# Optimization experiments

Measured on AMD Instinct MI355X. Metric: run time of the kernel, lower is better.

## Reference

```python
import jax, jax.numpy as jnp
import numpy as np

N_ITER = 3
B, L, U = 32, 120, 640
INPUT_CAPS = 32 * 9 * 12  # 3456
N_CLASSES = 5
FINAL_DIM = 16
N_REL = 25


def squash(x):
    # x: (B, n_caps, dim); squash along dim (axis=2)
    l2 = jnp.sum(x * x, axis=2, keepdims=True)
    return x * (l2 / (1.0 + l2) / jnp.sqrt(l2))


def conv2d(x, w, b, stride):
    out = jax.lax.conv_general_dilated(
        x, w, window_strides=stride, padding='VALID',
        dimension_numbers=('NCHW', 'OIHW', 'NCHW'))
    return out + b[None, :, None, None]


def setup_inputs() -> dict:
    key = jax.random.key(0)
    ks = jax.random.split(key, 10)
    stdv = 1.0 / np.sqrt(INPUT_CAPS)
    return {
        'input': jax.random.normal(ks[0], (B, 1, L, U), jnp.float32),
        'conv1_w': jax.random.normal(ks[1], (256, 1, L // 4, U // 4), jnp.float32) * 0.02,
        'conv1_b': jnp.zeros((256,), jnp.float32),
        'prim_w': jax.random.normal(ks[2], (256, 256, 10, 10), jnp.float32) * 0.02,
        'prim_b': jnp.zeros((256,), jnp.float32),
        'caps_w': jax.random.uniform(ks[3], (INPUT_CAPS, 8, N_CLASSES * FINAL_DIM),
                                     jnp.float32, -stdv, stdv),
        'b_route': jnp.zeros((INPUT_CAPS, N_CLASSES), jnp.float32),
        'pred_w': jax.random.normal(ks[4], (N_REL, FINAL_DIM), jnp.float32) * 0.1,
        'pred_b': jnp.zeros((N_REL,), jnp.float32),
        'eos_w': jax.random.normal(ks[5], (1, FINAL_DIM), jnp.float32) * 0.1,
        'eos_b': jnp.zeros((1,), jnp.float32),
    }


def reference(input, conv1_w, conv1_b, prim_w, prim_b, caps_w, b_route,
              pred_w, pred_b, eos_w, eos_b):
    # conv1 + relu: (B,1,120,640) -> (B,256,91,121)
    x = jax.nn.relu(conv2d(input, conv1_w, conv1_b, (1, 4)))
    # primary caps conv: -> (B,256,9,12)
    out = conv2d(x, prim_w, prim_b, (10, 10))
    n, _, h, w = out.shape
    out = out.reshape(n, 32, 8, h, w)                 # (B,32,8,9,12)
    out = jnp.transpose(out, (0, 1, 3, 4, 2))         # (B,32,9,12,8)
    u = squash(out.reshape(n, -1, 8))                 # (B,3456,8)
    # caps layer prediction: (B,I,8) x (I,8,O*D) -> (B,I,O,D)
    u_predict = jnp.einsum('bic,icj->bij', u, caps_w)
    u_predict = u_predict.reshape(n, INPUT_CAPS, N_CLASSES, FINAL_DIM)
    # agreement routing
    c = jax.nn.softmax(b_route, axis=1)               # (I,O)
    s = jnp.einsum('io,biod->bod', c, u_predict)
    v = squash(s)
    b_batch = jnp.broadcast_to(b_route, (n, INPUT_CAPS, N_CLASSES))
    for _ in range(N_ITER):
        b_batch = b_batch + jnp.einsum('biod,bod->bio', u_predict, v)
        c = jax.nn.softmax(b_batch, axis=-1)          # (B,I,O)
        s = jnp.einsum('bio,biod->bod', c, u_predict)
        v = squash(s)                                 # (B,O,D)
    predict_logits = v @ pred_w.T + pred_b            # (B,O,25)
    eos_logits = v @ eos_w.T + eos_b                  # (B,O,1)
    logits = jnp.concatenate([predict_logits, eos_logits], axis=-1)
    return jax.nn.log_softmax(logits, axis=-1)
```

## Files before the change

kernel.cpp:

```cpp
#include <hip/hip_runtime.h>

typedef __bf16 bf16x8 __attribute__((ext_vector_type(8)));
typedef __bf16 bf16x4 __attribute__((ext_vector_type(4)));
typedef float  f32x4  __attribute__((ext_vector_type(4)));
typedef unsigned int  uint;
typedef unsigned short ushort_t;

static __device__ __forceinline__ ushort_t f2bf(float f) {
    uint u = __float_as_uint(f);
    return (ushort_t)((u + 0x7fffu + ((u >> 16) & 1u)) >> 16);
}
static __device__ __forceinline__ float bf2f(ushort_t u) {
    return __uint_as_float((uint)u << 16);
}
static __device__ __forceinline__ f32x4 up4(uint2 p) {
    f32x4 r;
    r[0] = __uint_as_float(p.x << 16);
    r[1] = __uint_as_float(p.x & 0xffff0000u);
    r[2] = __uint_as_float(p.y << 16);
    r[3] = __uint_as_float(p.y & 0xffff0000u);
    return r;
}


constexpr size_t OFF_W1F = 0;
constexpr size_t SZ_W1F  = (size_t)256 * 4800 * 2;
constexpr size_t OFF_A2  = OFF_W1F + SZ_W1F;
constexpr size_t SZ_A2   = (size_t)256 * 25600 * 2;
constexpr size_t OFF_X   = OFF_A2 + SZ_A2;
constexpr size_t SZ_X    = (size_t)32 * 90 * 120 * 256 * 2;
constexpr size_t OFF_P   = OFF_X + SZ_X;
constexpr size_t SZ_P    = (size_t)8 * 256 * 32 * 112 * 2;
constexpr size_t OFF_UP  = OFF_X;
constexpr size_t OFF_BB  = OFF_X + (size_t)24 * 1024 * 1024;
constexpr size_t OFF_S0  = OFF_X + (size_t)28 * 1024 * 1024;
constexpr size_t OFF_S1  = OFF_X + (size_t)29 * 1024 * 1024;
constexpr size_t WS_NEED = OFF_P + SZ_P;

__global__ void k0_w1(const float* __restrict__ w, ushort_t* __restrict__ o) {
    int t = blockIdx.x * 256 + threadIdx.x;
    int l   = t & 63;
    int q   = t >> 6;
    int kwc = q % 5;
    int ocb = (q / 5) % 16;
    int kh  = q / 80;
    const float* src = w + (size_t)(ocb * 16 + (l & 15)) * 4800 + kh * 160 + kwc * 32 + (l >> 4) * 8;
    float4 f0 = *(const float4*)src;
    float4 f1 = *(const float4*)(src + 4);
    uint4 pk;
    pk.x = (uint)f2bf(f0.x) | ((uint)f2bf(f0.y) << 16);
    pk.y = (uint)f2bf(f0.z) | ((uint)f2bf(f0.w) << 16);
    pk.z = (uint)f2bf(f1.x) | ((uint)f2bf(f1.y) << 16);
    pk.w = (uint)f2bf(f1.z) | ((uint)f2bf(f1.w) << 16);
    *(uint4*)&o[(size_t)t * 8] = pk;
}

__global__ void k0_a2(const float* __restrict__ w, ushort_t* __restrict__ o) {
    __shared__ ushort_t l[25600];
    int oc2 = blockIdx.x;
    const float* src = w + (size_t)oc2 * 25600;
    for (int idx = threadIdx.x; idx < 25600; idx += 256) l[idx] = f2bf(src[idx]);
    __syncthreads();
    ushort_t* dst = o + (size_t)oc2 * 25600;
    for (int idx = threadIdx.x; idx < 25600; idx += 256) {
        int p = idx >> 8, ic = idx & 255;
        dst[idx] = l[ic * 100 + p];
    }
}

__global__ __launch_bounds__(256, 2) void k1_conv1(const float* __restrict__ inp,
                                                   const ushort_t* __restrict__ w1f,
                                                   const float* __restrict__ cb,
                                                   ushort_t* __restrict__ X) {
    __shared__ ushort_t smem[31680];
    ushort_t* brow = smem;
    const int tid = threadIdx.x, lane = tid & 63, wid = tid >> 6;
    const int wm = wid * 64;
    const int h = blockIdx.x, b = blockIdx.y;
    const int l16 = lane & 15, g8 = (lane >> 4) * 8;
    const int bbase = 4 * l16 + g8;
    f32x4 acc[4][8] = {};

    for (int idx = tid; idx < 5280; idx += 256) {
        int r = idx / 176, c = idx % 176;
        uint2 pk; pk.x = 0u; pk.y = 0u;
        if (c < 160) {
            const float* irow = inp + ((size_t)b * 120 + h + r) * 640;
            float4 f = *(const float4*)&irow[c * 4];
            pk.x = (uint)f2bf(f.x) | ((uint)f2bf(f.y) << 16);
            pk.y = (uint)f2bf(f.z) | ((uint)f2bf(f.w) << 16);
        }
        *(uint2*)&brow[r * 704 + c * 4] = pk;
    }
    __syncthreads();

#pragma unroll 1
    for (int kh = 0; kh < 30; ++kh) {
        bf16x8 bc[19];
        const int rb = kh * 704 + bbase;
#pragma unroll
        for (int t = 0; t < 19; ++t) {
            union { bf16x8 v8; bf16x4 v4[2]; } fr;
            fr.v4[0] = *(const bf16x4*)&brow[rb + 32 * t];
            fr.v4[1] = *(const bf16x4*)&brow[rb + 32 * t + 4];
            bc[t] = fr.v8;
        }
#pragma unroll
        for (int kwc = 0; kwc < 5; ++kwc) {
            bf16x8 af[4];
#pragma unroll
            for (int mt = 0; mt < 4; ++mt) {
                int q = (kh * 16 + wid * 4 + mt) * 5 + kwc;
                af[mt] = *(const bf16x8*)&w1f[(size_t)q * 512 + lane * 8];
            }
#pragma unroll
            for (int nt = 0; nt < 8; ++nt)
#pragma unroll
                for (int mt = 0; mt < 4; ++mt)
                    acc[mt][nt] = __builtin_amdgcn_mfma_f32_16x16x32_bf16(af[mt], bc[2 * nt + kwc], acc[mt][nt], 0, 0, 0);
        }
    }

    float cbv[4][4];
#pragma unroll
    for (int mt = 0; mt < 4; ++mt)
#pragma unroll
        for (int r = 0; r < 4; ++r)
            cbv[mt][r] = cb[wm + mt * 16 + (lane >> 4) * 4 + r];
    __syncthreads();
    ushort_t* cs = smem;
#pragma unroll
    for (int nt = 0; nt < 8; ++nt) {
        int wg = nt * 16 + l16;
        if (wg < 120) {
#pragma unroll
            for (int mt = 0; mt < 4; ++mt)
#pragma unroll
                for (int r = 0; r < 4; ++r) {
                    int oc = wm + mt * 16 + (lane >> 4) * 4 + r;
                    float v = acc[mt][nt][r] + cbv[mt][r];
                    v = v > 0.f ? v : 0.f;
                    cs[wg * 264 + oc] = f2bf(v);
                }
        }
    }
    __syncthreads();
    ushort_t* Xbase = X + ((size_t)b * 90 + h) * 120 * 256;
    for (int idx = tid; idx < 3840; idx += 256) {
        int w = idx >> 5, c = (idx & 31) * 8;
        *(uint4*)&Xbase[(size_t)w * 256 + c] = *(const uint4*)&cs[w * 264 + c];
    }
}

__global__ __launch_bounds__(512) void k2_prim(const ushort_t* __restrict__ X,
                                               const ushort_t* __restrict__ A2,
                                               ushort_t* __restrict__ P) {
    __shared__ float red[4][64][57];
    const int tid = threadIdx.x, lane = tid & 63, wid = tid >> 6;
    const int half = wid >> 2, ws2 = wid & 3;
    const int mi = blockIdx.x, s = blockIdx.y, b = blockIdx.z;
    const int msub = mi * 128 + ws2 * 32;
    const int l16 = lane & 15, g8 = (lane >> 4) * 8;
    f32x4 acc[2][7] = {};
    size_t aoff[2];
#pragma unroll
    for (int t = 0; t < 2; ++t) aoff[t] = (size_t)(msub + t * 16 + l16) * 25600 + g8;
    size_t noff[7];
#pragma unroll
    for (int nt = 0; nt < 7; ++nt) {
        int n = nt * 16 + l16; n = n < 108 ? n : 107;
        int h2 = n / 12, w2 = n % 12;
        noff[nt] = (((size_t)b * 90 + 10 * h2) * 120 + 10 * w2) * 256 + g8;
    }
    const int pbeg = (100 * s) / 8, pend = (100 * (s + 1)) / 8;
    const int pmid = pbeg + (pend - pbeg + 1) / 2;
    const int p0 = half ? pmid : pbeg;
    const int p1 = half ? pend : pmid;
#pragma unroll 1
    for (int p = p0; p < p1; ++p) {
        int ph = p / 10, pw = p % 10;
        size_t xb = (size_t)(ph * 120 + pw) * 256;
        size_t ab = (size_t)p * 256;
#pragma unroll
        for (int icc = 0; icc < 8; ++icc) {
            bf16x8 af[2], bfr[7];
#pragma unroll
            for (int t = 0; t < 2; ++t)
                af[t] = *(const bf16x8*)&A2[aoff[t] + ab + icc * 32];
#pragma unroll
            for (int nt = 0; nt < 7; ++nt)
                bfr[nt] = *(const bf16x8*)&X[noff[nt] + xb + icc * 32];
#pragma unroll
            for (int t = 0; t < 2; ++t)
#pragma unroll
                for (int nt = 0; nt < 7; ++nt)
                    acc[t][nt] = __builtin_amdgcn_mfma_f32_16x16x32_bf16(af[t], bfr[nt], acc[t][nt], 0, 0, 0);
        }
    }
    if (half == 1) {
#pragma unroll
        for (int t = 0; t < 2; ++t)
#pragma unroll
            for (int nt = 0; nt < 7; ++nt)
#pragma unroll
                for (int r = 0; r < 4; ++r)
                    red[ws2][lane][(t * 7 + nt) * 4 + r] = acc[t][nt][r];
    }
    __syncthreads();
    if (half == 0) {
#pragma unroll
        for (int t = 0; t < 2; ++t)
#pragma unroll
            for (int nt = 0; nt < 7; ++nt)
#pragma unroll
                for (int r = 0; r < 4; ++r) {
                    float v = acc[t][nt][r] + red[ws2][lane][(t * 7 + nt) * 4 + r];
                    int n   = nt * 16 + l16;
                    int oc2 = msub + t * 16 + (lane >> 4) * 4 + r;
                    P[(((size_t)s * 256 + oc2) * 32 + b) * 112 + n] = f2bf(v);
                }
    }
}

__global__ __launch_bounds__(128) void k3_caps(const ushort_t* __restrict__ P,
                                               const float* __restrict__ prim_b,
                                               const float* __restrict__ caps_w,
                                               ushort_t* __restrict__ UP) {
    const int b = blockIdx.x;
    const int i = blockIdx.y * 128 + threadIdx.x;
    const int cap = i / 108, hw = i % 108;
    float ud[8], l2 = 0.f;
#pragma unroll
    for (int d = 0; d < 8; ++d) {
        int oc2 = cap * 8 + d;
        float v = prim_b[oc2];
#pragma unroll
        for (int s = 0; s < 8; ++s)
            v += bf2f(P[(((size_t)s * 256 + oc2) * 32 + b) * 112 + hw]);
        ud[d] = v; l2 += v * v;
    }
    float scale = sqrtf(l2) / (1.f + l2);
#pragma unroll
    for (int d = 0; d < 8; ++d) ud[d] *= scale;
    const float* cw = caps_w + (size_t)i * 640;
    ushort_t* up = UP + ((size_t)b * 3456 + i) * 80;
    for (int j = 0; j < 80; j += 4) {
        f32x4 o = {0.f, 0.f, 0.f, 0.f};
#pragma unroll
        for (int d = 0; d < 8; ++d) {
            f32x4 w = *(const f32x4*)&cw[d * 80 + j];
            o += ud[d] * w;
        }
        uint2 pk;
        pk.x = (uint)f2bf(o[0]) | ((uint)f2bf(o[1]) << 16);
        pk.y = (uint)f2bf(o[2]) | ((uint)f2bf(o[3]) << 16);
        *(uint2*)&up[j] = pk;
    }
}

__global__ __launch_bounds__(128) void k4_iter(const ushort_t* __restrict__ UP,
                                               const float* __restrict__ b_route,
                                               float* __restrict__ BB,
                                               const float* __restrict__ spIn,
                                               float* __restrict__ spOut,
                                               int flags) {
    __shared__ __attribute__((aligned(16))) float sv[80];
    __shared__ float sred[2][80];
    __shared__ float sscale[5];
    const int tid = threadIdx.x, lane = tid & 63, wv = tid >> 6;
    const int chunk = blockIdx.x, b = blockIdx.y;

    if (flags & 1) {
        if (tid < 80) {
            float s = 0.f;
            for (int c2 = 0; c2 < 27; ++c2) s += spIn[((size_t)b * 27 + c2) * 80 + tid];
            sv[tid] = s;
        }
        __syncthreads();
        if (tid < 5) {
            float l2 = 0.f;
            for (int d = 0; d < 16; ++d) { float x = sv[tid * 16 + d]; l2 += x * x; }
            sscale[tid] = sqrtf(l2) / (1.f + l2);
        }
        __syncthreads();
        if (tid < 80) sv[tid] *= sscale[tid / 16];
    }
    __syncthreads();

    const int i = chunk * 128 + tid;
    const ushort_t* up = UP + ((size_t)b * 3456 + i) * 80;
    f32x4 u4[20];
#pragma unroll
    for (int r = 0; r < 20; ++r) u4[r] = up4(*(const uint2*)&up[r * 4]);

    float bo[5];
#pragma unroll
    for (int o = 0; o < 5; ++o) {
        float bv = (flags & 2) ? BB[((size_t)b * 3456 + i) * 5 + o] : b_route[i * 5 + o];
        if (flags & 1) {
            f32x4 dv = u4[o * 4 + 0] * (*(const f32x4*)&sv[o * 16 + 0])
                     + u4[o * 4 + 1] * (*(const f32x4*)&sv[o * 16 + 4])
                     + u4[o * 4 + 2] * (*(const f32x4*)&sv[o * 16 + 8])
                     + u4[o * 4 + 3] * (*(const f32x4*)&sv[o * 16 + 12]);
            bv += dv[0] + dv[1] + dv[2] + dv[3];
        }
        if (flags & 4) BB[((size_t)b * 3456 + i) * 5 + o] = bv;
        bo[o] = bv;
    }
    float m = fmaxf(fmaxf(fmaxf(bo[0], bo[1]), fmaxf(bo[2], bo[3])), bo[4]);
    float e[5], sum = 0.f;
#pragma unroll
    for (int o = 0; o < 5; ++o) { e[o] = __expf(bo[o] - m); sum += e[o]; }
    float inv = 1.f / sum;
    f32x4 a4[20];
#pragma unroll
    for (int o = 0; o < 5; ++o) {
        float c = e[o] * inv;
#pragma unroll
        for (int q = 0; q < 4; ++q) a4[o * 4 + q] = c * u4[o * 4 + q];
    }
#pragma unroll
    for (int off = 32; off >= 1; off >>= 1)
#pragma unroll
        for (int q = 0; q < 20; ++q)
#pragma unroll
            for (int c = 0; c < 4; ++c) a4[q][c] += __shfl_xor(a4[q][c], off, 64);
    if (lane == 0)
#pragma unroll
        for (int q = 0; q < 20; ++q)
#pragma unroll
            for (int c = 0; c < 4; ++c) sred[wv][q * 4 + c] = a4[q][c];
    __syncthreads();
    if (tid < 80) spOut[((size_t)b * 27 + chunk) * 80 + tid] = sred[0][tid] + sred[1][tid];
}

__global__ __launch_bounds__(192) void k4_fin(const float* __restrict__ spIn,
                                              const float* __restrict__ pred_w,
                                              const float* __restrict__ pred_b,
                                              const float* __restrict__ eos_w,
                                              const float* __restrict__ eos_b,
                                              float* __restrict__ out) {
    __shared__ __attribute__((aligned(16))) float sv[80];
    __shared__ float sscale[5];
    __shared__ float lg[130];
    __shared__ float lse[5];
    const int tid = threadIdx.x, b = blockIdx.x;
    if (tid < 80) {
        float s = 0.f;
        for (int c2 = 0; c2 < 27; ++c2) s += spIn[((size_t)b * 27 + c2) * 80 + tid];
        sv[tid] = s;
    }
    __syncthreads();
    if (tid < 5) {
        float l2 = 0.f;
        for (int d = 0; d < 16; ++d) { float x = sv[tid * 16 + d]; l2 += x * x; }
        sscale[tid] = sqrtf(l2) / (1.f + l2);
    }
    __syncthreads();
    if (tid < 80) sv[tid] *= sscale[tid / 16];
    __syncthreads();
    if (tid < 130) {
        int o = tid / 26, j = tid % 26;
        const float* wv = (j < 25) ? &pred_w[j * 16] : &eos_w[0];
        float dot = (j < 25) ? pred_b[j] : eos_b[0];
        for (int d = 0; d < 16; ++d) dot += sv[o * 16 + d] * wv[d];
        lg[tid] = dot;
    }
    __syncthreads();
    if (tid < 5) {
        float m = lg[tid * 26];
        for (int j = 1; j < 26; ++j) m = fmaxf(m, lg[tid * 26 + j]);
        float sum = 0.f;
        for (int j = 0; j < 26; ++j) sum += expf(lg[tid * 26 + j] - m);
        lse[tid] = m + logf(sum);
    }
    __syncthreads();
    if (tid < 130) out[b * 130 + tid] = lg[tid] - lse[tid / 26];
}

extern "C" void kernel_launch(void* const* d_in, const int* in_sizes, int n_in,
                              void* d_out, int out_size, void* d_ws, size_t ws_size,
                              hipStream_t stream) {
    const float* inp    = (const float*)d_in[0];
    const float* w1     = (const float*)d_in[1];
    const float* cb1    = (const float*)d_in[2];
    const float* w2     = (const float*)d_in[3];
    const float* pb2    = (const float*)d_in[4];
    const float* capsw  = (const float*)d_in[5];
    const float* broute = (const float*)d_in[6];
    const float* predw  = (const float*)d_in[7];
    const float* predb  = (const float*)d_in[8];
    const float* eosw   = (const float*)d_in[9];
    const float* eosb   = (const float*)d_in[10];
    float* out = (float*)d_out;
    char* ws = (char*)d_ws;
    if (ws_size < WS_NEED) return;

    ushort_t* w1f = (ushort_t*)(ws + OFF_W1F);
    ushort_t* a2  = (ushort_t*)(ws + OFF_A2);
    ushort_t* X   = (ushort_t*)(ws + OFF_X);
    ushort_t* P   = (ushort_t*)(ws + OFF_P);
    ushort_t* UP  = (ushort_t*)(ws + OFF_UP);
    float*    BB  = (float*)(ws + OFF_BB);
    float*    S0  = (float*)(ws + OFF_S0);
    float*    S1  = (float*)(ws + OFF_S1);

    k0_w1   <<<dim3(600),      dim3(256), 0, stream>>>(w1, w1f);
    k0_a2   <<<dim3(256),      dim3(256), 0, stream>>>(w2, a2);
    k1_conv1<<<dim3(90, 32),   dim3(256), 0, stream>>>(inp, w1f, cb1, X);
    k2_prim <<<dim3(2, 8, 32), dim3(512), 0, stream>>>(X, a2, P);
    k3_caps <<<dim3(32, 27),   dim3(128), 0, stream>>>(P, pb2, capsw, UP);
    k4_iter <<<dim3(27, 32),   dim3(128), 0, stream>>>(UP, broute, BB, S1, S0, 0);
    k4_iter <<<dim3(27, 32),   dim3(128), 0, stream>>>(UP, broute, BB, S0, S1, 1 | 4);
    k4_iter <<<dim3(27, 32),   dim3(128), 0, stream>>>(UP, broute, BB, S1, S0, 1 | 2 | 4);
    k4_iter <<<dim3(27, 32),   dim3(128), 0, stream>>>(UP, broute, BB, S0, S1, 1 | 2);
    k4_fin  <<<dim3(32),       dim3(192), 0, stream>>>(S1, predw, predb, eosw, eosb, out);
}
```

Before: 1.062 ms.

## Drop intra-block split-K in primary conv and remap caps threads by batch

The primary-capsule conv kernel no longer splits each block's K range across two half-blocks and then reduces them through shared memory. Each 256-thread block now runs the whole K slice itself and writes P directly, which removes the LDS buffer and the barrier but halves the number of waves working on each block. The caps kernel is relaunched as a flat 1D grid with batch in the low 5 bits of the thread index, so the 32 threads sharing a capsule read the same caps_w row, while P and UP accesses become strided across batch.

```diff
diff --git a/kernel.cpp b/kernel.cpp
--- a/kernel.cpp
+++ b/kernel.cpp
@@ -152,14 +152,12 @@
     }
 }
 
-__global__ __launch_bounds__(512) void k2_prim(const ushort_t* __restrict__ X,
+__global__ __launch_bounds__(256) void k2_prim(const ushort_t* __restrict__ X,
                                                const ushort_t* __restrict__ A2,
                                                ushort_t* __restrict__ P) {
-    __shared__ float red[4][64][57];
     const int tid = threadIdx.x, lane = tid & 63, wid = tid >> 6;
-    const int half = wid >> 2, ws2 = wid & 3;
     const int mi = blockIdx.x, s = blockIdx.y, b = blockIdx.z;
-    const int msub = mi * 128 + ws2 * 32;
+    const int msub = mi * 128 + wid * 32;
     const int l16 = lane & 15, g8 = (lane >> 4) * 8;
     f32x4 acc[2][7] = {};
     size_t aoff[2];
@@ -172,10 +170,7 @@
         int h2 = n / 12, w2 = n % 12;
         noff[nt] = (((size_t)b * 90 + 10 * h2) * 120 + 10 * w2) * 256 + g8;
     }
-    const int pbeg = (100 * s) / 8, pend = (100 * (s + 1)) / 8;
-    const int pmid = pbeg + (pend - pbeg + 1) / 2;
-    const int p0 = half ? pmid : pbeg;
-    const int p1 = half ? pend : pmid;
+    const int p0 = (100 * s) / 8, p1 = (100 * (s + 1)) / 8;
 #pragma unroll 1
     for (int p = p0; p < p1; ++p) {
         int ph = p / 10, pw = p % 10;
@@ -197,38 +192,25 @@
                     acc[t][nt] = __builtin_amdgcn_mfma_f32_16x16x32_bf16(af[t], bfr[nt], acc[t][nt], 0, 0, 0);
         }
     }
-    if (half == 1) {
-#pragma unroll
-        for (int t = 0; t < 2; ++t)
-#pragma unroll
-            for (int nt = 0; nt < 7; ++nt)
-#pragma unroll
-                for (int r = 0; r < 4; ++r)
-                    red[ws2][lane][(t * 7 + nt) * 4 + r] = acc[t][nt][r];
-    }
-    __syncthreads();
-    if (half == 0) {
-#pragma unroll
-        for (int t = 0; t < 2; ++t)
-#pragma unroll
-            for (int nt = 0; nt < 7; ++nt)
-#pragma unroll
-                for (int r = 0; r < 4; ++r) {
-                    float v = acc[t][nt][r] + red[ws2][lane][(t * 7 + nt) * 4 + r];
-                    int n   = nt * 16 + l16;
-                    int oc2 = msub + t * 16 + (lane >> 4) * 4 + r;
-                    P[(((size_t)s * 256 + oc2) * 32 + b) * 112 + n] = f2bf(v);
-                }
-    }
-}
-
-__global__ __launch_bounds__(128) void k3_caps(const ushort_t* __restrict__ P,
+#pragma unroll
+    for (int t = 0; t < 2; ++t)
+#pragma unroll
+        for (int nt = 0; nt < 7; ++nt)
+#pragma unroll
+            for (int r = 0; r < 4; ++r) {
+                int n   = nt * 16 + l16;
+                int oc2 = msub + t * 16 + (lane >> 4) * 4 + r;
+                P[(((size_t)s * 256 + oc2) * 32 + b) * 112 + n] = f2bf(acc[t][nt][r]);
+            }
+}
+
+__global__ __launch_bounds__(256) void k3_caps(const ushort_t* __restrict__ P,
                                                const float* __restrict__ prim_b,
                                                const float* __restrict__ caps_w,
                                                ushort_t* __restrict__ UP) {
-    const int b = blockIdx.x;
-    const int i = blockIdx.y * 128 + threadIdx.x;
-    const int cap = i / 108, hw = i % 108;
+    int t = blockIdx.x * 256 + threadIdx.x;
+    int b = t & 31, i = t >> 5;
+    int cap = i / 108, hw = i % 108;
     float ud[8], l2 = 0.f;
 #pragma unroll
     for (int d = 0; d < 8; ++d) {
@@ -408,8 +390,8 @@
     k0_w1   <<<dim3(600),      dim3(256), 0, stream>>>(w1, w1f);
     k0_a2   <<<dim3(256),      dim3(256), 0, stream>>>(w2, a2);
     k1_conv1<<<dim3(90, 32),   dim3(256), 0, stream>>>(inp, w1f, cb1, X);
-    k2_prim <<<dim3(2, 8, 32), dim3(512), 0, stream>>>(X, a2, P);
-    k3_caps <<<dim3(32, 27),   dim3(128), 0, stream>>>(P, pb2, capsw, UP);
+    k2_prim <<<dim3(2, 8, 32), dim3(256), 0, stream>>>(X, a2, P);
+    k3_caps <<<dim3(432),      dim3(256), 0, stream>>>(P, pb2, capsw, UP);
     k4_iter <<<dim3(27, 32),   dim3(128), 0, stream>>>(UP, broute, BB, S1, S0, 0);
     k4_iter <<<dim3(27, 32),   dim3(128), 0, stream>>>(UP, broute, BB, S0, S1, 1 | 4);
     k4_iter <<<dim3(27, 32),   dim3(128), 0, stream>>>(UP, broute, BB, S1, S0, 1 | 2 | 4);
```

Result: faster. 1.033 ms (median of 2 runs) (-2.7%).
